# Optimization experiments

Hardware: AMD Instinct MI355X
Metric: run time of the kernel (lower is better)

Reference implementation:

```python
import jax, jax.numpy as jnp
import numpy as np

B, S, D, H = 2, 2048, 2048, 16
HD = D // H  # head_dim = 128

def _rope_tables(head_dim, context_length, theta_base=10000.0):
    inv_freq = 1.0 / theta_base ** (jnp.arange(0, head_dim, 2, dtype=jnp.float32) / head_dim)
    pos = jnp.arange(context_length, dtype=jnp.float32)
    angles = pos[:, None] * inv_freq[None, :]            # [S, HD/2]
    angles = jnp.concatenate([angles, angles], axis=1)   # [S, HD]
    return jnp.cos(angles), jnp.sin(angles)

def _apply_rope(x, cos, sin):
    # x: [b, h, s, hd]; cos/sin: [s, hd]
    hd = x.shape[-1]
    x1, x2 = x[..., : hd // 2], x[..., hd // 2 :]
    rotated = jnp.concatenate([-x2, x1], axis=-1)
    return x * cos[None, None] + rotated * sin[None, None]

def setup_inputs() -> dict:
    key = jax.random.key(0)
    ks = jax.random.split(key, 5)
    x = jax.random.normal(ks[0], (B, S, D), dtype=jnp.float32)
    scale = 1.0 / np.sqrt(D)
    Wq = jax.random.normal(ks[1], (D, D), dtype=jnp.float32) * scale
    Wk = jax.random.normal(ks[2], (D, D), dtype=jnp.float32) * scale
    Wv = jax.random.normal(ks[3], (D, D), dtype=jnp.float32) * scale
    Wo = jax.random.normal(ks[4], (D, D), dtype=jnp.float32) * scale
    cos, sin = _rope_tables(HD, S)
    return {"x": x, "Wq": Wq, "Wk": Wk, "Wv": Wv, "Wo": Wo, "cos": cos, "sin": sin}

def reference(x, Wq, Wk, Wv, Wo, cos, sin):
    b, s, _ = x.shape
    def split_heads(t):  # [b,s,D] -> [b,H,s,HD]
        return t.reshape(b, s, H, HD).transpose(0, 2, 1, 3)
    q = split_heads(x @ Wq.T)
    k = split_heads(x @ Wk.T)
    v = split_heads(x @ Wv.T)
    q = _apply_rope(q, cos[:s], sin[:s])
    k = _apply_rope(k, cos[:s], sin[:s])
    scores = jnp.einsum("bhqd,bhkd->bhqk", q, k) / np.sqrt(HD)
    causal = jnp.triu(jnp.ones((s, s), dtype=bool), k=1)
    scores = jnp.where(causal[None, None], -jnp.inf, scores)
    weights = jax.nn.softmax(scores, axis=-1)
    ctx = jnp.einsum("bhqk,bhkd->bhqd", weights, v)
    ctx = ctx.transpose(0, 2, 1, 3).reshape(b, s, D)
    return ctx @ Wo.T
```

## Files before the change

kernel.cpp:

```cpp
#include <hip/hip_runtime.h>
#include <cstdint>
#include <cmath>

#define B_ 2
#define S_ 2048
#define D_ 2048
#define H_ 16
#define HD_ 128

#define NEG_SENTINEL -1.0e30f

typedef __bf16 bf16;
typedef __attribute__((ext_vector_type(4))) __bf16 bf16x4;
typedef __attribute__((ext_vector_type(8))) __bf16 bf16x8;
typedef __attribute__((ext_vector_type(4))) float f32x4;

__device__ __forceinline__ void gload_lds16(const void* g, void* l) {
  __builtin_amdgcn_global_load_lds(
      (const __attribute__((address_space(1))) unsigned int*)g,
      (__attribute__((address_space(3))) unsigned int*)l, 16, 0, 0);
}

__device__ __forceinline__ f32x4 mfma16(bf16x8 a, bf16x8 b, f32x4 c) {
  return __builtin_amdgcn_mfma_f32_16x16x32_bf16(a, b, c, 0, 0, 0);
}

__global__ __launch_bounds__(256) void cvt_f32_bf16(
    const float* __restrict__ in, bf16* __restrict__ out)
{
  int i = blockIdx.x * 256 + threadIdx.x;
  f32x4 v = ((const f32x4*)in)[i];
  bf16x4 o;
#pragma unroll
  for (int j = 0; j < 4; ++j) o[j] = (bf16)v[j];
  ((bf16x4*)out)[i] = o;
}

#define GTM 128
#define GTN 128
#define GBK 64

template <typename OT>
__global__ __launch_bounds__(256) void gemm_xwt(
    const bf16* __restrict__ A, const bf16* __restrict__ W, OT* __restrict__ C,
    int M, int N, int K, int ldc)
{
  __shared__ bf16 sA[GTM * GBK];
  __shared__ bf16 sB[GTN * GBK];
  const int tid  = threadIdx.x;
  const int wave = tid >> 6, lane = tid & 63;
  const int quad = lane >> 4, l16 = lane & 15;
  const int tm = blockIdx.y * GTM;
  const int tn = blockIdx.x * GTN;
  const int wm = (wave >> 1) * 64, wn = (wave & 1) * 64;

  f32x4 acc[4][4];
#pragma unroll
  for (int i = 0; i < 4; ++i)
#pragma unroll
    for (int j = 0; j < 4; ++j) acc[i][j] = (f32x4)0.0f;

  for (int k0 = 0; k0 < K; k0 += GBK) {
    __syncthreads();
#pragma unroll
    for (int g = 0; g < 4; ++g) {
      int gb  = (g * 4 + wave) * 64;
      int p   = gb + lane;
      int row = p >> 3, pos = p & 7;
      int cc  = pos ^ (row & 7);
      gload_lds16(A + (size_t)(tm + row) * K + k0 + cc * 8, (char*)sA + (size_t)gb * 16);
      gload_lds16(W + (size_t)(tn + row) * K + k0 + cc * 8, (char*)sB + (size_t)gb * 16);
    }
    __syncthreads();

#pragma unroll
    for (int t = 0; t < 2; ++t) {
      bf16x8 af[4], bfr[4];
#pragma unroll
      for (int i = 0; i < 4; ++i) {
        int rowa = wm + i * 16 + l16;
        int posa = (t * 4 + quad) ^ (rowa & 7);
        af[i] = *(const bf16x8*)(sA + rowa * GBK + posa * 8);
        int rowb = wn + i * 16 + l16;
        int posb = (t * 4 + quad) ^ (rowb & 7);
        bfr[i] = *(const bf16x8*)(sB + rowb * GBK + posb * 8);
      }
#pragma unroll
      for (int i = 0; i < 4; ++i)
#pragma unroll
        for (int j = 0; j < 4; ++j)
          acc[i][j] = mfma16(af[i], bfr[j], acc[i][j]);
    }
  }

#pragma unroll
  for (int i = 0; i < 4; ++i)
#pragma unroll
    for (int r = 0; r < 4; ++r) {
      int row = tm + wm + i * 16 + quad * 4 + r;
#pragma unroll
      for (int j = 0; j < 4; ++j) {
        int col = tn + wn + j * 16 + l16;
        C[(size_t)row * ldc + col] = (OT)acc[i][j][r];
      }
    }
}

__global__ __launch_bounds__(256) void rope_qk(
    bf16* __restrict__ Q, bf16* __restrict__ Kk,
    const float* __restrict__ cosT, const float* __restrict__ sinT, int rs)
{
  const float kappa = 0.08838834764831845f * 1.4426950408889634f;
  int t = blockIdx.x * 256 + threadIdx.x;
  int d = t & 63;
  int h = (t >> 6) & (H_ - 1);
  int s = (t >> 10) & (S_ - 1);
  int b = t >> 21;
  size_t base = ((size_t)(b * S_ + s)) * rs + (size_t)h * HD_;
  float c1 = cosT[s * HD_ + d];
  float s1 = sinT[s * HD_ + d];
  float c2 = cosT[s * HD_ + d + 64];
  float s2 = sinT[s * HD_ + d + 64];
  {
    float x1 = (float)Q[base + d], x2 = (float)Q[base + d + 64];
    Q[base + d]      = (bf16)((x1 * c1 - x2 * s1) * kappa);
    Q[base + d + 64] = (bf16)((x2 * c2 + x1 * s2) * kappa);
  }
  {
    float x1 = (float)Kk[base + d], x2 = (float)Kk[base + d + 64];
    Kk[base + d]      = (bf16)(x1 * c1 - x2 * s1);
    Kk[base + d + 64] = (bf16)(x2 * c2 + x1 * s2);
  }
}

__global__ __launch_bounds__(256) void transpose_v(
    const bf16* __restrict__ V, bf16* __restrict__ Vt, int rs)
{
  __shared__ bf16 sT[64 * 72];
  const int tid = threadIdx.x;
  const int si = blockIdx.x;
  const int di = blockIdx.y;
  const int bh = blockIdx.z;
  const int b  = bh >> 4, h = bh & 15;

  const bf16* src = V + (size_t)b * S_ * rs + (size_t)h * HD_ + di * 64;
  bf16*       dst = Vt + ((size_t)bh * HD_ + di * 64) * S_ + si * 64;

#pragma unroll
  for (int half = 0; half < 2; ++half) {
    int r  = half * 32 + (tid >> 3);
    int c0 = (tid & 7) * 8;
    bf16x8 v = *(const bf16x8*)(src + (size_t)(si * 64 + r) * rs + c0);
    *(bf16x8*)(sT + r * 72 + c0) = v;
  }
  __syncthreads();
#pragma unroll
  for (int half = 0; half < 2; ++half) {
    int dr = half * 32 + (tid >> 3);
    int c0 = (tid & 7) * 8;
    bf16x8 o;
#pragma unroll
    for (int j = 0; j < 8; ++j) o[j] = sT[(c0 + j) * 72 + dr];
    *(bf16x8*)(dst + (size_t)dr * S_ + c0) = o;
  }
}

#define ABK 64
#define SPS 72

__global__ __launch_bounds__(256) void attn_fwd(
    const bf16* __restrict__ Q, const bf16* __restrict__ K,
    const bf16* __restrict__ Vt, bf16* __restrict__ O, int rs)
{
  __shared__ bf16 sK[ABK * HD_];
  __shared__ bf16 sVT[HD_ * ABK];
  __shared__ bf16 sP[64 * SPS];

  const int tid  = threadIdx.x;
  const int wave = tid >> 6, lane = tid & 63;
  const int quad = lane >> 4, l16 = lane & 15;

  const int lin   = (int)blockIdx.x;
  const int low3  = lin & 7;
  const int rest  = lin >> 3;
  const int pairx = rest & 15;
  const int colhi = rest >> 4;
  const int col   = low3 + (colhi << 3);
  const int b = col >> 4, h = col & 15;

  const bf16* Qh  = Q + (size_t)b * S_ * rs + (size_t)h * HD_;
  const bf16* Kh  = K + (size_t)b * S_ * rs + (size_t)h * HD_;
  const bf16* Vth = Vt + ((size_t)(b * H_ + h) * HD_) * S_;
  bf16*       Oh  = O + (size_t)b * S_ * D_ + (size_t)h * HD_;

  const int wq = wave * 16;

#pragma unroll 1
  for (int seg = 0; seg < 2; ++seg) {
    const int qt = seg == 0 ? pairx : 31 - pairx;
    const int q0 = qt * 64;
    const int wq_abs = q0 + wq;

    bf16x8 qf[4];
    {
      const bf16* rp = Qh + (size_t)(wq_abs + l16) * rs + quad * 8;
#pragma unroll
      for (int t = 0; t < 4; ++t) qf[t] = *(const bf16x8*)(rp + t * 32);
    }

    f32x4 o_acc[8];
#pragma unroll
    for (int j = 0; j < 8; ++j) o_acc[j] = (f32x4)0.0f;
    float m_col = NEG_SENTINEL;
    float l_col = 0.0f;

    const int nkt = qt + 1;
#pragma unroll 1
    for (int kt = 0; kt < nkt; ++kt) {
      const int kk0 = kt * ABK;
      __syncthreads();

#pragma unroll
      for (int g = 0; g < 4; ++g) {
        int p   = g * 256 + tid;
        int row = p >> 4, pos = p & 15;
        int cc  = pos ^ (row & 15);
        gload_lds16(Kh + (size_t)(kk0 + row) * rs + cc * 8, (char*)sK + (size_t)p * 16);
      }
#pragma unroll
      for (int g = 0; g < 4; ++g) {
        int p  = g * 256 + tid;
        int d  = p >> 3, pos = p & 7;
        int cc = pos ^ (d & 7);
        gload_lds16(Vth + (size_t)d * S_ + kk0 + cc * 8, (char*)sVT + (size_t)p * 16);
      }
      __syncthreads();

      if (kk0 <= wq_abs + 15) {
        f32x4 st[4];
#pragma unroll
        for (int jt = 0; jt < 4; ++jt) {
          bf16x8 kf[4];
#pragma unroll
          for (int t = 0; t < 4; ++t) {
            int pos = (t * 4 + quad) ^ l16;
            kf[t] = *(const bf16x8*)(sK + (jt * 16 + l16) * HD_ + pos * 8);
          }
          f32x4 a = (f32x4)0.0f;
#pragma unroll
          for (int t = 0; t < 4; ++t) a = mfma16(kf[t], qf[t], a);
          st[jt] = a;
        }

        if (kk0 + 63 > wq_abs) {
          int qcol = wq_abs + l16;
#pragma unroll
          for (int jt = 0; jt < 4; ++jt)
#pragma unroll
            for (int r = 0; r < 4; ++r) {
              int key = kk0 + jt * 16 + quad * 4 + r;
              if (key > qcol) st[jt][r] = NEG_SENTINEL;
            }
        }

        float mx = NEG_SENTINEL;
#pragma unroll
        for (int jt = 0; jt < 4; ++jt)
#pragma unroll
          for (int r = 0; r < 4; ++r) mx = fmaxf(mx, st[jt][r]);
        mx = fmaxf(mx, __shfl_xor(mx, 16, 64));
        mx = fmaxf(mx, __shfl_xor(mx, 32, 64));
        float m_new = fmaxf(m_col, mx);
        float alpha = exp2f(m_col - m_new);
        float ts = 0.0f;
#pragma unroll
        for (int jt = 0; jt < 4; ++jt) {
          bf16x4 pk;
#pragma unroll
          for (int r = 0; r < 4; ++r) {
            float p = exp2f(st[jt][r] - m_new);
            ts += p;
            pk[r] = (bf16)p;
          }
          *(bf16x4*)(sP + (wq + l16) * SPS + jt * 16 + quad * 4) = pk;
        }
        ts += __shfl_xor(ts, 16, 64);
        ts += __shfl_xor(ts, 32, 64);
        l_col = l_col * alpha + ts;
        m_col = m_new;
#pragma unroll
        for (int r = 0; r < 4; ++r) {
          float av = __shfl(alpha, quad * 4 + r, 64);
#pragma unroll
          for (int jd = 0; jd < 8; ++jd) o_acc[jd][r] *= av;
        }

#pragma unroll
        for (int ks = 0; ks < 2; ++ks) {
          bf16x8 pf = *(const bf16x8*)(sP + (wq + l16) * SPS + ks * 32 + quad * 8);
#pragma unroll
          for (int jd = 0; jd < 8; ++jd) {
            int pos = (ks * 4 + quad) ^ (l16 & 7);
            bf16x8 vf = *(const bf16x8*)(sVT + (jd * 16 + l16) * ABK + pos * 8);
            o_acc[jd] = mfma16(pf, vf, o_acc[jd]);
          }
        }
      }
    }

#pragma unroll
    for (int r = 0; r < 4; ++r) {
      float lv = __shfl(l_col, quad * 4 + r, 64);
      float inv_l = 1.0f / lv;
      int row = wq_abs + quad * 4 + r;
#pragma unroll
      for (int jd = 0; jd < 8; ++jd) {
        int colo = jd * 16 + l16;
        Oh[(size_t)row * D_ + colo] = (bf16)(o_acc[jd][r] * inv_l);
      }
    }
  }
}

extern "C" void kernel_launch(void* const* d_in, const int* in_sizes, int n_in,
                              void* d_out, int out_size, void* d_ws, size_t ws_size,
                              hipStream_t stream) {
  const float* x    = (const float*)d_in[0];
  const float* Wq   = (const float*)d_in[1];
  const float* Wk   = (const float*)d_in[2];
  const float* Wv   = (const float*)d_in[3];
  const float* Wo   = (const float*)d_in[4];
  const float* cosT = (const float*)d_in[5];
  const float* sinT = (const float*)d_in[6];
  float* out = (float*)d_out;

  const size_t NE = (size_t)B_ * S_ * D_;
  const size_t WE = (size_t)D_ * D_;
  const int M = B_ * S_;
  const int cvtX = (int)(NE / 1024);
  const int cvtW = (int)(WE / 1024);

  if (ws_size >= (size_t)92274688) {
    bf16* QKV   = (bf16*)d_ws;
    bf16* xb    = QKV + (size_t)M * 6144;
    bf16* Wqkv  = xb + NE;
    bf16* ctx   = Wqkv;
    bf16* Wob   = Wqkv + 2 * WE;
    bf16* Vt    = xb;

    cvt_f32_bf16<<<cvtX, 256, 0, stream>>>(x, xb);
    cvt_f32_bf16<<<cvtW, 256, 0, stream>>>(Wq, Wqkv);
    cvt_f32_bf16<<<cvtW, 256, 0, stream>>>(Wk, Wqkv + WE);
    cvt_f32_bf16<<<cvtW, 256, 0, stream>>>(Wv, Wqkv + 2 * WE);
    gemm_xwt<bf16><<<dim3(48, 32), 256, 0, stream>>>(xb, Wqkv, QKV, M, 3 * D_, D_, 3 * D_);
    rope_qk<<<(B_ * S_ * H_ * 64) / 256, 256, 0, stream>>>(QKV, QKV + D_, cosT, sinT, 3 * D_);
    transpose_v<<<dim3(32, 2, 32), 256, 0, stream>>>(QKV + 2 * D_, Vt, 3 * D_);
    attn_fwd<<<512, 256, 0, stream>>>(QKV, QKV + D_, Vt, ctx, 3 * D_);
    cvt_f32_bf16<<<cvtW, 256, 0, stream>>>(Wo, Wob);
    gemm_xwt<float><<<dim3(16, 32), 256, 0, stream>>>(ctx, Wob, out, M, D_, D_, D_);
  } else {
    bf16* Qb    = (bf16*)d_ws;
    bf16* Kb    = Qb + NE;
    bf16* Vb    = Kb + NE;
    bf16* Cb    = Vb + NE;
    bf16* Wslot = Cb + NE;

    cvt_f32_bf16<<<cvtX, 256, 0, stream>>>(x, Cb);
    cvt_f32_bf16<<<cvtW, 256, 0, stream>>>(Wq, Wslot);
    gemm_xwt<bf16><<<dim3(16, 32), 256, 0, stream>>>(Cb, Wslot, Qb, M, D_, D_, D_);
    cvt_f32_bf16<<<cvtW, 256, 0, stream>>>(Wk, Wslot);
    gemm_xwt<bf16><<<dim3(16, 32), 256, 0, stream>>>(Cb, Wslot, Kb, M, D_, D_, D_);
    cvt_f32_bf16<<<cvtW, 256, 0, stream>>>(Wv, Wslot);
    gemm_xwt<bf16><<<dim3(16, 32), 256, 0, stream>>>(Cb, Wslot, Vb, M, D_, D_, D_);
    rope_qk<<<(B_ * S_ * H_ * 64) / 256, 256, 0, stream>>>(Qb, Kb, cosT, sinT, D_);
    transpose_v<<<dim3(32, 2, 32), 256, 0, stream>>>(Vb, Cb, D_);
    attn_fwd<<<512, 256, 0, stream>>>(Qb, Kb, Cb, Vb, D_);
    cvt_f32_bf16<<<cvtW, 256, 0, stream>>>(Wo, Wslot);
    gemm_xwt<float><<<dim3(16, 32), 256, 0, stream>>>(Vb, Wslot, out, M, D_, D_, D_);
  }
}
```

Before: 402.8 us.

## Load K/V directly from global in attention and fuse input conversions

Attention stops staging K and V^T tiles in shared memory and has each wave read its MFMA fragments straight from global memory. This removes the two block barriers per key tile. The per-wave causal skip check is also dropped, so fully masked tiles are computed but contribute zero. The four fp32-to-bf16 conversion launches are merged into one kernel to cut launch overhead. The risk is that K/V reuse across waves now depends on caches, and global fragment loads are less coalesced.

```diff
diff --git a/kernel.cpp b/kernel.cpp
--- a/kernel.cpp
+++ b/kernel.cpp
@@ -33,6 +33,28 @@
   bf16x4 o;
 #pragma unroll
   for (int j = 0; j < 4; ++j) o[j] = (bf16)v[j];
+  ((bf16x4*)out)[i] = o;
+}
+
+__global__ __launch_bounds__(256) void cvt_qkvx(
+    const float* __restrict__ x, bf16* __restrict__ xb,
+    const float* __restrict__ wq, const float* __restrict__ wk,
+    const float* __restrict__ wv, bf16* __restrict__ wout)
+{
+  int b = (int)blockIdx.x;
+  const float* in; bf16* out; int base;
+  if (b < 8192)      { in = x;  out = xb; base = b; }
+  else {
+    int r = b - 8192; int j = r >> 12; base = r & 4095;
+    if (j == 0)      { in = wq; out = wout; }
+    else if (j == 1) { in = wk; out = wout + 4194304; }
+    else             { in = wv; out = wout + 8388608; }
+  }
+  int i = base * 256 + threadIdx.x;
+  f32x4 v = ((const f32x4*)in)[i];
+  bf16x4 o;
+#pragma unroll
+  for (int t2 = 0; t2 < 4; ++t2) o[t2] = (bf16)v[t2];
   ((bf16x4*)out)[i] = o;
 }
 
@@ -172,8 +194,6 @@
     const bf16* __restrict__ Q, const bf16* __restrict__ K,
     const bf16* __restrict__ Vt, bf16* __restrict__ O, int rs)
 {
-  __shared__ bf16 sK[ABK * HD_];
-  __shared__ bf16 sVT[HD_ * ABK];
   __shared__ bf16 sP[64 * SPS];
 
   const int tid  = threadIdx.x;
@@ -218,92 +238,72 @@
 #pragma unroll 1
     for (int kt = 0; kt < nkt; ++kt) {
       const int kk0 = kt * ABK;
-      __syncthreads();
-
-#pragma unroll
-      for (int g = 0; g < 4; ++g) {
-        int p   = g * 256 + tid;
-        int row = p >> 4, pos = p & 15;
-        int cc  = pos ^ (row & 15);
-        gload_lds16(Kh + (size_t)(kk0 + row) * rs + cc * 8, (char*)sK + (size_t)p * 16);
-      }
-#pragma unroll
-      for (int g = 0; g < 4; ++g) {
-        int p  = g * 256 + tid;
-        int d  = p >> 3, pos = p & 7;
-        int cc = pos ^ (d & 7);
-        gload_lds16(Vth + (size_t)d * S_ + kk0 + cc * 8, (char*)sVT + (size_t)p * 16);
-      }
-      __syncthreads();
-
-      if (kk0 <= wq_abs + 15) {
-        f32x4 st[4];
-#pragma unroll
-        for (int jt = 0; jt < 4; ++jt) {
-          bf16x8 kf[4];
-#pragma unroll
-          for (int t = 0; t < 4; ++t) {
-            int pos = (t * 4 + quad) ^ l16;
-            kf[t] = *(const bf16x8*)(sK + (jt * 16 + l16) * HD_ + pos * 8);
+
+      f32x4 st[4];
+#pragma unroll
+      for (int jt = 0; jt < 4; ++jt) {
+        const bf16* krow = Kh + (size_t)(kk0 + jt * 16 + l16) * rs;
+        bf16x8 kf[4];
+#pragma unroll
+        for (int t = 0; t < 4; ++t)
+          kf[t] = *(const bf16x8*)(krow + (t * 4 + quad) * 8);
+        f32x4 a2 = (f32x4)0.0f;
+#pragma unroll
+        for (int t = 0; t < 4; ++t) a2 = mfma16(kf[t], qf[t], a2);
+        st[jt] = a2;
+      }
+
+      if (kk0 + 63 > wq_abs) {
+        int qcol = wq_abs + l16;
+#pragma unroll
+        for (int jt = 0; jt < 4; ++jt)
+#pragma unroll
+          for (int r = 0; r < 4; ++r) {
+            int key = kk0 + jt * 16 + quad * 4 + r;
+            if (key > qcol) st[jt][r] = NEG_SENTINEL;
           }
-          f32x4 a = (f32x4)0.0f;
-#pragma unroll
-          for (int t = 0; t < 4; ++t) a = mfma16(kf[t], qf[t], a);
-          st[jt] = a;
+      }
+
+      float mx = NEG_SENTINEL;
+#pragma unroll
+      for (int jt = 0; jt < 4; ++jt)
+#pragma unroll
+        for (int r = 0; r < 4; ++r) mx = fmaxf(mx, st[jt][r]);
+      mx = fmaxf(mx, __shfl_xor(mx, 16, 64));
+      mx = fmaxf(mx, __shfl_xor(mx, 32, 64));
+      float m_new = fmaxf(m_col, mx);
+      float alpha = exp2f(m_col - m_new);
+      float ts = 0.0f;
+#pragma unroll
+      for (int jt = 0; jt < 4; ++jt) {
+        bf16x4 pk;
+#pragma unroll
+        for (int r = 0; r < 4; ++r) {
+          float p = exp2f(st[jt][r] - m_new);
+          ts += p;
+          pk[r] = (bf16)p;
         }
-
-        if (kk0 + 63 > wq_abs) {
-          int qcol = wq_abs + l16;
-#pragma unroll
-          for (int jt = 0; jt < 4; ++jt)
-#pragma unroll
-            for (int r = 0; r < 4; ++r) {
-              int key = kk0 + jt * 16 + quad * 4 + r;
-              if (key > qcol) st[jt][r] = NEG_SENTINEL;
-            }
-        }
-
-        float mx = NEG_SENTINEL;
-#pragma unroll
-        for (int jt = 0; jt < 4; ++jt)
-#pragma unroll
-          for (int r = 0; r < 4; ++r) mx = fmaxf(mx, st[jt][r]);
-        mx = fmaxf(mx, __shfl_xor(mx, 16, 64));
-        mx = fmaxf(mx, __shfl_xor(mx, 32, 64));
-        float m_new = fmaxf(m_col, mx);
-        float alpha = exp2f(m_col - m_new);
-        float ts = 0.0f;
-#pragma unroll
-        for (int jt = 0; jt < 4; ++jt) {
-          bf16x4 pk;
-#pragma unroll
-          for (int r = 0; r < 4; ++r) {
-            float p = exp2f(st[jt][r] - m_new);
-            ts += p;
-            pk[r] = (bf16)p;
-          }
-          *(bf16x4*)(sP + (wq + l16) * SPS + jt * 16 + quad * 4) = pk;
-        }
-        ts += __shfl_xor(ts, 16, 64);
-        ts += __shfl_xor(ts, 32, 64);
-        l_col = l_col * alpha + ts;
-        m_col = m_new;
-#pragma unroll
-        for (int r = 0; r < 4; ++r) {
-          float av = __shfl(alpha, quad * 4 + r, 64);
-#pragma unroll
-          for (int jd = 0; jd < 8; ++jd) o_acc[jd][r] *= av;
-        }
-
-#pragma unroll
-        for (int ks = 0; ks < 2; ++ks) {
-          bf16x8 pf = *(const bf16x8*)(sP + (wq + l16) * SPS + ks * 32 + quad * 8);
-#pragma unroll
-          for (int jd = 0; jd < 8; ++jd) {
-            int pos = (ks * 4 + quad) ^ (l16 & 7);
-            bf16x8 vf = *(const bf16x8*)(sVT + (jd * 16 + l16) * ABK + pos * 8);
-            o_acc[jd] = mfma16(pf, vf, o_acc[jd]);
-          }
+        *(bf16x4*)(sP + (wq + l16) * SPS + jt * 16 + quad * 4) = pk;
+      }
+      ts += __shfl_xor(ts, 16, 64);
+      ts += __shfl_xor(ts, 32, 64);
+      l_col = l_col * alpha + ts;
+      m_col = m_new;
+#pragma unroll
+      for (int r = 0; r < 4; ++r) {
+        float av = __shfl(alpha, quad * 4 + r, 64);
+#pragma unroll
+        for (int jd = 0; jd < 8; ++jd) o_acc[jd][r] *= av;
+      }
+
+#pragma unroll
+      for (int ks = 0; ks < 2; ++ks) {
+        bf16x8 pf = *(const bf16x8*)(sP + (wq + l16) * SPS + ks * 32 + quad * 8);
+#pragma unroll
+        for (int jd = 0; jd < 8; ++jd) {
+          const bf16* vrow = Vth + (size_t)(jd * 16 + l16) * S_ + kk0;
+          bf16x8 vf = *(const bf16x8*)(vrow + (ks * 4 + quad) * 8);
+          o_acc[jd] = mfma16(pf, vf, o_acc[jd]);
         }
       }
     }
@@ -348,10 +348,7 @@
     bf16* Wob   = Wqkv + 2 * WE;
     bf16* Vt    = xb;
 
-    cvt_f32_bf16<<<cvtX, 256, 0, stream>>>(x, xb);
-    cvt_f32_bf16<<<cvtW, 256, 0, stream>>>(Wq, Wqkv);
-    cvt_f32_bf16<<<cvtW, 256, 0, stream>>>(Wk, Wqkv + WE);
-    cvt_f32_bf16<<<cvtW, 256, 0, stream>>>(Wv, Wqkv + 2 * WE);
+    cvt_qkvx<<<8192 + 3 * 4096, 256, 0, stream>>>(x, xb, Wq, Wk, Wv, Wqkv);
     gemm_xwt<bf16><<<dim3(48, 32), 256, 0, stream>>>(xb, Wqkv, QKV, M, 3 * D_, D_, 3 * D_);
     rope_qk<<<(B_ * S_ * H_ * 64) / 256, 256, 0, stream>>>(QKV, QKV + D_, cosT, sinT, 3 * D_);
     transpose_v<<<dim3(32, 2, 32), 256, 0, stream>>>(QKV + 2 * D_, Vt, 3 * D_);
```

Result: slower. 554.5 us (+37.7%).
